# Kernel optimization log

Measured on AMD Instinct MI355X. Metric: run time of the kernel, lower is better.

## Reference

```python
import jax, jax.numpy as jnp
import numpy as np

B, P, T, D = 8192, 64, 406, 10
NUM_CLASSES = 19


def setup_inputs() -> dict:
    key = jax.random.key(0)
    k1, k2, k3, k4 = jax.random.split(key, 4)
    input_seq = jax.random.normal(k1, (B, T, D), dtype=jnp.float32)
    label = jax.random.randint(k2, (B,), 0, NUM_CLASSES, dtype=jnp.int64)
    # binary observation mask (float, multiplicative) as in the torch module
    mask = (jax.random.uniform(k3, (B, T)) > 0.1).astype(jnp.float32)
    prototypes = jax.random.normal(k4, (P, T, D), dtype=jnp.float32)
    return {"input_seq": input_seq, "label": label, "mask": mask, "prototypes": prototypes}


def reference(input_seq, label, mask, prototypes):
    # Masked squared distance: d[b,p] = sum_{t,d} mask[b,t] * (x[b,t,d] - c[p,t,d])^2
    # Expanded so the [B,P,T,D] broadcast tensor is never materialized:
    #   = sum m*x^2  - 2 * sum m*x*c  + sum m*c^2
    mx = input_seq * mask[..., None]                                  # [B,T,D]
    sq_x = jnp.einsum('btd,btd->b', mx, input_seq)                    # [B]
    cross = jnp.einsum('btd,ptd->bp', mx, prototypes)                 # [B,P]
    sq_p = jnp.einsum('bt,ptd->bp', mask, prototypes * prototypes)    # [B,P]
    distances = sq_x[:, None] - 2.0 * cross + sq_p                    # [B,P]
    indices = jnp.argmin(distances, axis=1)                           # [B]
    output_seq = prototypes[indices]                                  # [B,T,D] gather
    return (output_seq, input_seq, distances, indices, label, mask)
```

## Files before the change

kernel.cpp:

```cpp
#include <hip/hip_runtime.h>

#define B_   8192
#define T_   406
#define D_   10
#define P_   64
#define K0_  4060
#define KE_  4466
#define KP_  4480
#define NKS_ 8

#define OUT_SEQ   0
#define OUT_IN    (B_*T_*D_)
#define OUT_DIST  (2*B_*T_*D_)
#define OUT_IDX   (OUT_DIST + B_*P_)
#define OUT_LAB   (OUT_IDX + B_)
#define OUT_MASK  (OUT_LAB + B_)

typedef unsigned short ushort_t;
typedef __attribute__((ext_vector_type(8))) short bf16x8;
typedef __attribute__((ext_vector_type(4))) float f32x4;
typedef __attribute__((address_space(3))) unsigned int lds_uint;
typedef __attribute__((address_space(1))) unsigned int glb_uint;

__device__ __forceinline__ void gl_lds16(const void* g, void* l) {
    __builtin_amdgcn_global_load_lds((const glb_uint*)g, (lds_uint*)l, 16, 0, 0);
}
__device__ __forceinline__ ushort_t f2bf(float f) {
    unsigned u = __float_as_uint(f);
    return (ushort_t)((u + 0x7fffu + ((u >> 16) & 1u)) >> 16);
}

__global__ __launch_bounds__(256) void k0_prep(
    const float* __restrict__ x, const float* __restrict__ mask,
    ushort_t* __restrict__ axb, float* __restrict__ out_in,
    float* __restrict__ out_mask, float* __restrict__ sq_x)
{
    __shared__ float ms[4][416];
    const int wave = threadIdx.x >> 6, lane = threadIdx.x & 63;
    const int row = blockIdx.x * 4 + wave;
    const float* mrow = mask + (size_t)row * T_;
    float* omrow = out_mask + (size_t)row * T_;
    for (int j = lane; j < T_; j += 64) { float m = mrow[j]; ms[wave][j] = m; omrow[j] = m; }
    const float4* x4 = (const float4*)(x + (size_t)row * K0_);
    float4* o4 = (float4*)(out_in + (size_t)row * K0_);
    ushort_t* arow = axb + (size_t)row * KP_;
    const int rk = row & 7;
    float sx = 0.f;
    for (int i = lane; i < 1015; i += 64) {
        float4 v = x4[i];
        o4[i] = v;
        int k = 4 * i;
        int t0 = (k*6554)>>16, t1 = ((k+1)*6554)>>16;
        int t2 = ((k+2)*6554)>>16, t3 = ((k+3)*6554)>>16;
        float a0 = v.x * ms[wave][t0], a1 = v.y * ms[wave][t1];
        float a2 = v.z * ms[wave][t2], a3 = v.w * ms[wave][t3];
        sx += a0*v.x + a1*v.y + a2*v.z + a3*v.w;
        int c = i >> 1;
        int s = (c & ~7) | ((c ^ rk) & 7);
        ushort4 w; w.x = f2bf(a0); w.y = f2bf(a1); w.z = f2bf(a2); w.w = f2bf(a3);
        *(ushort4*)(arow + s * 8 + (i & 1) * 4) = w;
    }
    for (int i = 1015 + lane; i < 1120; i += 64) {
        int k = 4 * i;
        ushort4 w;
        w.x = (k     < KE_) ? f2bf(ms[wave][k     - K0_]) : (ushort_t)0;
        w.y = (k + 1 < KE_) ? f2bf(ms[wave][k + 1 - K0_]) : (ushort_t)0;
        w.z = (k + 2 < KE_) ? f2bf(ms[wave][k + 2 - K0_]) : (ushort_t)0;
        w.w = (k + 3 < KE_) ? f2bf(ms[wave][k + 3 - K0_]) : (ushort_t)0;
        int c = i >> 1;
        int s = (c & ~7) | ((c ^ rk) & 7);
        *(ushort4*)(arow + s * 8 + (i & 1) * 4) = w;
    }
#pragma unroll
    for (int off = 32; off >= 1; off >>= 1) sx += __shfl_xor(sx, off, 64);
    if (lane == 0) sq_x[row] = sx;
}

__global__ __launch_bounds__(256) void k1_prep(
    const float* __restrict__ protos, ushort_t* __restrict__ bxb)
{
    const int p = blockIdx.x;
    const int rk = p & 7;
    ushort_t* brow = bxb + (size_t)p * KP_;
    for (int t = threadIdx.x; t < T_; t += 256) {
        const float* src = protos + (size_t)p * K0_ + t * 10;
        float s2 = 0.f;
#pragma unroll
        for (int d = 0; d < 10; d++) {
            float c = src[d];
            s2 += c * c;
            int k = t * 10 + d;
            int ch = k >> 3;
            int sw = (ch & ~7) | ((ch ^ rk) & 7);
            brow[sw * 8 + (k & 7)] = f2bf(-2.f * c);
        }
        int k = K0_ + t;
        int ch = k >> 3;
        int sw = (ch & ~7) | ((ch ^ rk) & 7);
        brow[sw * 8 + (k & 7)] = f2bf(s2);
    }
    for (int k = KE_ + (int)threadIdx.x; k < KP_; k += 256) {
        int ch = k >> 3;
        int sw = (ch & ~7) | ((ch ^ rk) & 7);
        brow[sw * 8 + (k & 7)] = 0;
    }
}

__global__ __launch_bounds__(256) void k2_gemm(
    const ushort_t* __restrict__ axb, const ushort_t* __restrict__ bxb,
    float* __restrict__ partial)
{
    __shared__ ushort_t As[128 * 128];
    __shared__ ushort_t Bs[64 * 128];
    const int tid = threadIdx.x, wave = tid >> 6, lane = tid & 63;
    const int mb = blockIdx.x >> 3, ks = blockIdx.x & 7;
    const int rowBase = mb * 128;
    const int cstart = ks * 4 + (ks < 3 ? ks : 3);
    const int ccnt = (ks < 3) ? 5 : 4;
    const int mh = (wave & 1) * 64;
    const int nh = (wave >> 1) * 32;
    const int m16 = lane & 15, q4 = lane >> 4;
    const int srow4 = lane >> 4, scol = lane & 15;

    f32x4 acc[4][2];
#pragma unroll
    for (int a = 0; a < 4; a++)
#pragma unroll
        for (int bb = 0; bb < 2; bb++) acc[a][bb] = (f32x4)0.f;

    for (int cc = 0; cc < ccnt; cc++) {
        const int ch = cstart + cc;
        __syncthreads();
#pragma unroll
        for (int j = 0; j < 8; j++) {
            int r = wave * 32 + j * 4 + srow4;
            const ushort_t* g = axb + (size_t)(rowBase + r) * KP_ + (ch * 16 + scol) * 8;
            gl_lds16(g, &As[(wave * 32 + j * 4) * 128]);
        }
#pragma unroll
        for (int j = 0; j < 4; j++) {
            int r = wave * 16 + j * 4 + srow4;
            const ushort_t* g = bxb + (size_t)r * KP_ + (ch * 16 + scol) * 8;
            gl_lds16(g, &Bs[(wave * 16 + j * 4) * 128]);
        }
        __syncthreads();
#pragma unroll
        for (int k4 = 0; k4 < 4; k4++) {
            const int chk = k4 * 4 + q4;
            const int sw = (chk & ~7) | ((chk ^ m16) & 7);
            bf16x8 af[4], bfr[2];
#pragma unroll
            for (int mt = 0; mt < 4; mt++)
                af[mt] = *(const bf16x8*)&As[(mh + mt * 16 + m16) * 128 + sw * 8];
#pragma unroll
            for (int nt = 0; nt < 2; nt++)
                bfr[nt] = *(const bf16x8*)&Bs[(nh + nt * 16 + m16) * 128 + sw * 8];
#pragma unroll
            for (int mt = 0; mt < 4; mt++)
#pragma unroll
                for (int nt = 0; nt < 2; nt++)
                    acc[mt][nt] = __builtin_amdgcn_mfma_f32_16x16x32_bf16(
                        af[mt], bfr[nt], acc[mt][nt], 0, 0, 0);
        }
    }
#pragma unroll
    for (int mt = 0; mt < 4; mt++)
#pragma unroll
        for (int nt = 0; nt < 2; nt++)
#pragma unroll
            for (int q = 0; q < 4; q++) {
                int gr = rowBase + mh + mt * 16 + q4 * 4 + q;
                int gp = nh + nt * 16 + m16;
                partial[((size_t)ks * B_ + gr) * P_ + gp] = acc[mt][nt][q];
            }
}

__global__ __launch_bounds__(256) void k3_fin(
    const float* __restrict__ partial, const float* __restrict__ sq_x,
    const float* __restrict__ protos, const int* __restrict__ label,
    float* __restrict__ out)
{
    __shared__ int sidx[4];
    const int tid = threadIdx.x, wave = tid >> 6, lane = tid & 63;
    const int b = blockIdx.x * 4 + wave;
    float v = sq_x[b];
#pragma unroll
    for (int ks = 0; ks < NKS_; ks++)
        v += partial[((size_t)ks * B_ + b) * P_ + lane];
    out[OUT_DIST + (size_t)b * 64 + lane] = v;

    float bv = v; int bi = lane;
#pragma unroll
    for (int off = 32; off >= 1; off >>= 1) {
        float ov = __shfl_xor(bv, off, 64);
        int   oi = __shfl_xor(bi, off, 64);
        if (ov < bv || (ov == bv && oi < bi)) { bv = ov; bi = oi; }
    }
    if (lane == 0) {
        sidx[wave] = bi;
        out[OUT_IDX + b] = (float)bi;
        out[OUT_LAB + b] = (float)label[b];
    }
    __syncthreads();
#pragma unroll
    for (int w2 = 0; w2 < 4; w2++) {
        const int bb = blockIdx.x * 4 + w2;
        const float* src = protos + (size_t)sidx[w2] * (T_ * D_);
        float* dst = out + OUT_SEQ + (size_t)bb * (T_ * D_);
        for (int i = tid; i < 1015; i += 256)
            *(float4*)(dst + 4 * i) = *(const float4*)(src + 4 * i);
    }
}

extern "C" void kernel_launch(void* const* d_in, const int* in_sizes, int n_in,
                              void* d_out, int out_size, void* d_ws, size_t ws_size,
                              hipStream_t stream) {
    const float* x      = (const float*)d_in[0];
    const int*   label  = (const int*)d_in[1];
    const float* mask   = (const float*)d_in[2];
    const float* protos = (const float*)d_in[3];
    float* out = (float*)d_out;
    char*  ws  = (char*)d_ws;

    ushort_t* bxb     = (ushort_t*)(ws);
    float*    sq_x    = (float*)(ws + 573440);
    float*    partial = (float*)(ws + 606208);
    ushort_t* axb     = (ushort_t*)(out + OUT_SEQ);

    hipLaunchKernelGGL(k0_prep, dim3(B_ / 4), dim3(256), 0, stream,
                       x, mask, axb, out + OUT_IN, out + OUT_MASK, sq_x);
    hipLaunchKernelGGL(k1_prep, dim3(64), dim3(256), 0, stream, protos, bxb);
    hipLaunchKernelGGL(k2_gemm, dim3(512), dim3(256), 0, stream, axb, bxb, partial);
    hipLaunchKernelGGL(k3_fin, dim3(B_ / 4), dim3(256), 0, stream,
                       partial, sq_x, protos, label, out);
}
```

Measured before the change: 448.8 us.

## Fuse input masking and bf16 conversion into the GEMM, dropping the prep kernel

The separate k0_prep kernel is removed. The GEMM now reads fp32 x and mask directly, applies the mask, accumulates sq_x, converts to bf16 in registers and writes it into the swizzled LDS tile. It also copies x and mask to the outputs and folds the per-row partial sq_x into each K-split partial. This avoids writing and rereading the bf16 A matrix through global memory, at the cost of synchronous register-staged loads in place of async global-to-LDS loads, and more per-thread ALU work inside the GEMM loop.

```diff
diff --git a/kernel.cpp b/kernel.cpp
--- a/kernel.cpp
+++ b/kernel.cpp
@@ -28,52 +28,6 @@
 __device__ __forceinline__ ushort_t f2bf(float f) {
     unsigned u = __float_as_uint(f);
     return (ushort_t)((u + 0x7fffu + ((u >> 16) & 1u)) >> 16);
-}
-
-__global__ __launch_bounds__(256) void k0_prep(
-    const float* __restrict__ x, const float* __restrict__ mask,
-    ushort_t* __restrict__ axb, float* __restrict__ out_in,
-    float* __restrict__ out_mask, float* __restrict__ sq_x)
-{
-    __shared__ float ms[4][416];
-    const int wave = threadIdx.x >> 6, lane = threadIdx.x & 63;
-    const int row = blockIdx.x * 4 + wave;
-    const float* mrow = mask + (size_t)row * T_;
-    float* omrow = out_mask + (size_t)row * T_;
-    for (int j = lane; j < T_; j += 64) { float m = mrow[j]; ms[wave][j] = m; omrow[j] = m; }
-    const float4* x4 = (const float4*)(x + (size_t)row * K0_);
-    float4* o4 = (float4*)(out_in + (size_t)row * K0_);
-    ushort_t* arow = axb + (size_t)row * KP_;
-    const int rk = row & 7;
-    float sx = 0.f;
-    for (int i = lane; i < 1015; i += 64) {
-        float4 v = x4[i];
-        o4[i] = v;
-        int k = 4 * i;
-        int t0 = (k*6554)>>16, t1 = ((k+1)*6554)>>16;
-        int t2 = ((k+2)*6554)>>16, t3 = ((k+3)*6554)>>16;
-        float a0 = v.x * ms[wave][t0], a1 = v.y * ms[wave][t1];
-        float a2 = v.z * ms[wave][t2], a3 = v.w * ms[wave][t3];
-        sx += a0*v.x + a1*v.y + a2*v.z + a3*v.w;
-        int c = i >> 1;
-        int s = (c & ~7) | ((c ^ rk) & 7);
-        ushort4 w; w.x = f2bf(a0); w.y = f2bf(a1); w.z = f2bf(a2); w.w = f2bf(a3);
-        *(ushort4*)(arow + s * 8 + (i & 1) * 4) = w;
-    }
-    for (int i = 1015 + lane; i < 1120; i += 64) {
-        int k = 4 * i;
-        ushort4 w;
-        w.x = (k     < KE_) ? f2bf(ms[wave][k     - K0_]) : (ushort_t)0;
-        w.y = (k + 1 < KE_) ? f2bf(ms[wave][k + 1 - K0_]) : (ushort_t)0;
-        w.z = (k + 2 < KE_) ? f2bf(ms[wave][k + 2 - K0_]) : (ushort_t)0;
-        w.w = (k + 3 < KE_) ? f2bf(ms[wave][k + 3 - K0_]) : (ushort_t)0;
-        int c = i >> 1;
-        int s = (c & ~7) | ((c ^ rk) & 7);
-        *(ushort4*)(arow + s * 8 + (i & 1) * 4) = w;
-    }
-#pragma unroll
-    for (int off = 32; off >= 1; off >>= 1) sx += __shfl_xor(sx, off, 64);
-    if (lane == 0) sq_x[row] = sx;
 }
 
 __global__ __launch_bounds__(256) void k1_prep(
@@ -106,13 +60,17 @@
     }
 }
 
-__global__ __launch_bounds__(256) void k2_gemm(
-    const ushort_t* __restrict__ axb, const ushort_t* __restrict__ bxb,
+__global__ __launch_bounds__(256) void k2_fused(
+    const float* __restrict__ x, const float* __restrict__ mask,
+    const ushort_t* __restrict__ bxb,
+    float* __restrict__ out_in, float* __restrict__ out_mask,
     float* __restrict__ partial)
 {
     __shared__ ushort_t As[128 * 128];
     __shared__ ushort_t Bs[64 * 128];
+    __shared__ float    sqs[128];
     const int tid = threadIdx.x, wave = tid >> 6, lane = tid & 63;
+    const int g = lane >> 4, c = lane & 15;
     const int mb = blockIdx.x >> 3, ks = blockIdx.x & 7;
     const int rowBase = mb * 128;
     const int cstart = ks * 4 + (ks < 3 ? ks : 3);
@@ -120,8 +78,18 @@
     const int mh = (wave & 1) * 64;
     const int nh = (wave >> 1) * 32;
     const int m16 = lane & 15, q4 = lane >> 4;
-    const int srow4 = lane >> 4, scol = lane & 15;
-
+
+    if (ks == 7) {
+        for (int r = wave; r < 128; r += 4) {
+            const float* mr = mask + (size_t)(rowBase + r) * T_;
+            float* omr = out_mask + (size_t)(rowBase + r) * T_;
+            for (int j = lane; j < T_; j += 64) omr[j] = mr[j];
+        }
+    }
+
+    float sqacc[8];
+#pragma unroll
+    for (int j = 0; j < 8; j++) sqacc[j] = 0.f;
     f32x4 acc[4][2];
 #pragma unroll
     for (int a = 0; a < 4; a++)
@@ -132,16 +100,76 @@
         const int ch = cstart + cc;
         __syncthreads();
 #pragma unroll
-        for (int j = 0; j < 8; j++) {
-            int r = wave * 32 + j * 4 + srow4;
-            const ushort_t* g = axb + (size_t)(rowBase + r) * KP_ + (ch * 16 + scol) * 8;
-            gl_lds16(g, &As[(wave * 32 + j * 4) * 128]);
-        }
-#pragma unroll
         for (int j = 0; j < 4; j++) {
-            int r = wave * 16 + j * 4 + srow4;
-            const ushort_t* g = bxb + (size_t)r * KP_ + (ch * 16 + scol) * 8;
-            gl_lds16(g, &Bs[(wave * 16 + j * 4) * 128]);
+            int r = wave * 16 + j * 4 + g;
+            const ushort_t* gb = bxb + (size_t)r * KP_ + (ch * 16 + c) * 8;
+            gl_lds16(gb, &Bs[(wave * 16 + j * 4) * 128]);
+        }
+        const int k8 = ch * 128 + c * 8;
+        if (ch < 31) {
+#pragma unroll
+            for (int j = 0; j < 8; j++) {
+                const int r = wave * 32 + j * 4 + g;
+                const size_t grow = (size_t)(rowBase + r);
+                const float* xr = x + grow * K0_ + k8;
+                float4 v0 = *(const float4*)xr;
+                float4 v1 = *(const float4*)(xr + 4);
+                float4* o = (float4*)(out_in + grow * K0_ + k8);
+                o[0] = v0; o[1] = v1;
+                int t0 = (k8 * 6554) >> 16;
+                int bnd = t0 * 10 + 10 - k8;
+                float m0 = mask[grow * T_ + t0];
+                float m1 = mask[grow * T_ + t0 + 1];
+                float a0 = v0.x * m0;
+                float a1 = v0.y * (1 < bnd ? m0 : m1);
+                float a2 = v0.z * (2 < bnd ? m0 : m1);
+                float a3 = v0.w * (3 < bnd ? m0 : m1);
+                float a4 = v1.x * (4 < bnd ? m0 : m1);
+                float a5 = v1.y * (5 < bnd ? m0 : m1);
+                float a6 = v1.z * (6 < bnd ? m0 : m1);
+                float a7 = v1.w * (7 < bnd ? m0 : m1);
+                sqacc[j] += a0 * v0.x + a1 * v0.y + a2 * v0.z + a3 * v0.w
+                          + a4 * v1.x + a5 * v1.y + a6 * v1.z + a7 * v1.w;
+                bf16x8 w;
+                w[0] = (short)f2bf(a0); w[1] = (short)f2bf(a1);
+                w[2] = (short)f2bf(a2); w[3] = (short)f2bf(a3);
+                w[4] = (short)f2bf(a4); w[5] = (short)f2bf(a5);
+                w[6] = (short)f2bf(a6); w[7] = (short)f2bf(a7);
+                const int sw = (c & ~7) | ((c ^ (r & 7)) & 7);
+                *(bf16x8*)&As[r * 128 + sw * 8] = w;
+            }
+        } else {
+#pragma unroll
+            for (int j = 0; j < 8; j++) {
+                const int r = wave * 32 + j * 4 + g;
+                const size_t grow = (size_t)(rowBase + r);
+                float av[8];
+#pragma unroll
+                for (int e = 0; e < 8; e++) {
+                    const int k = k8 + e;
+                    float a;
+                    if (k < K0_) {
+                        float xv = x[grow * K0_ + k];
+                        int t = (k * 6554) >> 16;
+                        float m = mask[grow * T_ + t];
+                        a = xv * m;
+                        out_in[grow * K0_ + k] = xv;
+                        sqacc[j] += a * xv;
+                    } else if (k < KE_) {
+                        a = mask[grow * T_ + (k - K0_)];
+                    } else {
+                        a = 0.f;
+                    }
+                    av[e] = a;
+                }
+                bf16x8 w;
+                w[0] = (short)f2bf(av[0]); w[1] = (short)f2bf(av[1]);
+                w[2] = (short)f2bf(av[2]); w[3] = (short)f2bf(av[3]);
+                w[4] = (short)f2bf(av[4]); w[5] = (short)f2bf(av[5]);
+                w[6] = (short)f2bf(av[6]); w[7] = (short)f2bf(av[7]);
+                const int sw = (c & ~7) | ((c ^ (r & 7)) & 7);
+                *(bf16x8*)&As[r * 128 + sw * 8] = w;
+            }
         }
         __syncthreads();
 #pragma unroll
@@ -164,26 +192,34 @@
         }
     }
 #pragma unroll
+    for (int j = 0; j < 8; j++) {
+#pragma unroll
+        for (int off = 8; off >= 1; off >>= 1)
+            sqacc[j] += __shfl_xor(sqacc[j], off, 64);
+        if (c == 0) sqs[wave * 32 + j * 4 + g] = sqacc[j];
+    }
+    __syncthreads();
+#pragma unroll
     for (int mt = 0; mt < 4; mt++)
 #pragma unroll
         for (int nt = 0; nt < 2; nt++)
 #pragma unroll
             for (int q = 0; q < 4; q++) {
-                int gr = rowBase + mh + mt * 16 + q4 * 4 + q;
+                int tr = mh + mt * 16 + q4 * 4 + q;
+                int gr = rowBase + tr;
                 int gp = nh + nt * 16 + m16;
-                partial[((size_t)ks * B_ + gr) * P_ + gp] = acc[mt][nt][q];
+                partial[((size_t)ks * B_ + gr) * P_ + gp] = acc[mt][nt][q] + sqs[tr];
             }
 }
 
 __global__ __launch_bounds__(256) void k3_fin(
-    const float* __restrict__ partial, const float* __restrict__ sq_x,
-    const float* __restrict__ protos, const int* __restrict__ label,
-    float* __restrict__ out)
+    const float* __restrict__ partial, const float* __restrict__ protos,
+    const int* __restrict__ label, float* __restrict__ out)
 {
     __shared__ int sidx[4];
     const int tid = threadIdx.x, wave = tid >> 6, lane = tid & 63;
     const int b = blockIdx.x * 4 + wave;
-    float v = sq_x[b];
+    float v = 0.f;
 #pragma unroll
     for (int ks = 0; ks < NKS_; ks++)
         v += partial[((size_t)ks * B_ + b) * P_ + lane];
@@ -223,14 +259,11 @@
     char*  ws  = (char*)d_ws;
 
     ushort_t* bxb     = (ushort_t*)(ws);
-    float*    sq_x    = (float*)(ws + 573440);
-    float*    partial = (float*)(ws + 606208);
-    ushort_t* axb     = (ushort_t*)(out + OUT_SEQ);
-
-    hipLaunchKernelGGL(k0_prep, dim3(B_ / 4), dim3(256), 0, stream,
-                       x, mask, axb, out + OUT_IN, out + OUT_MASK, sq_x);
+    float*    partial = (float*)(ws + 573440);
+
     hipLaunchKernelGGL(k1_prep, dim3(64), dim3(256), 0, stream, protos, bxb);
-    hipLaunchKernelGGL(k2_gemm, dim3(512), dim3(256), 0, stream, axb, bxb, partial);
+    hipLaunchKernelGGL(k2_fused, dim3(512), dim3(256), 0, stream,
+                       x, mask, bxb, out + OUT_IN, out + OUT_MASK, partial);
     hipLaunchKernelGGL(k3_fin, dim3(B_ / 4), dim3(256), 0, stream,
-                       partial, sq_x, protos, label, out);
-}
+                       partial, protos, label, out);
+}
```

Result: slower. 535.0 us (+19.2%).
